# Optimization experiments

Measured on AMD Instinct MI355X. Metric: run time of the kernel, lower is better.

## Reference

```python
import jax, jax.numpy as jnp
import numpy as np

N = 64
EPS = 1e-4
N_ITER = 100
BRANCH = 10


def setup_inputs() -> dict:
    key = jax.random.key(0)
    x = jax.random.normal(key, (8192, 4096), dtype=jnp.float32)
    return {"x": x}


def _lml(x):
    # x: [n_batch, nx], nx > N assumed (as configured in setup_inputs)
    n_batch, nx = x.shape
    x_sorted = jnp.sort(x, axis=1)[:, ::-1]  # descending
    nu_lower = -x_sorted[:, N - 1] - 7.0  # [n_batch]
    nu_upper = -x_sorted[:, N] + 7.0      # [n_batch]
    ls = jnp.linspace(0.0, 1.0, BRANCH).astype(x.dtype)  # [branch]
    rows = jnp.arange(n_batch)

    def cond(state):
        i, lo, hi = state
        return (i < N_ITER) & jnp.any(hi - lo > EPS)

    def body(state):
        i, lo, hi = state
        r = hi - lo                     # [n_batch]
        I = r > EPS                     # rows still being refined
        nus = r[:, None] * ls + lo[:, None]  # [n_batch, branch]
        # sigmoid-sum constraint at each candidate nu: [n_batch, branch]
        fs = jax.nn.sigmoid(x[:, None, :] + nus[:, :, None]).sum(axis=2) - N
        neg = (fs < 0).sum(axis=1) - 1  # index of last negative iterate
        J = neg < 0                     # all-positive-iterates warning case
        i_lower = jnp.clip(neg, 0, BRANCH - 2)
        new_lo = nus[rows, i_lower]
        new_hi = nus[rows, i_lower + 1]
        new_lo = jnp.where(J, new_lo - 7.0, new_lo)
        lo = jnp.where(I, new_lo, lo)
        hi = jnp.where(I, new_hi, hi)
        return i + 1, lo, hi

    _, lo, hi = jax.lax.while_loop(cond, body, (0, nu_lower, nu_upper))
    nu = lo + (hi - lo) / 2.0
    return jax.nn.sigmoid(x + nu[:, None])


def reference(x):
    return _lml(x)
```

## Files before the change

### kernel.cpp

```cpp
#include <hip/hip_runtime.h>

#define ROWLEN 4096
#define TPB    256
#define LOG2E  1.44269504088896340736f

typedef float f32x4 __attribute__((ext_vector_type(4)));

__device__ __forceinline__ float exp2_fast(float x) {
    float r; asm("v_exp_f32 %0, %1" : "=v"(r) : "v"(x)); return r;
}
__device__ __forceinline__ float rcp_fast(float x) {
    float r; asm("v_rcp_f32 %0, %1" : "=v"(r) : "v"(x)); return r;
}
__device__ __forceinline__ float log2_fast(float x) {
    float r; asm("v_log_f32 %0, %1" : "=v"(r) : "v"(x)); return r;
}
__device__ __forceinline__ float sqrt_fast(float x) {
    float r; asm("v_sqrt_f32 %0, %1" : "=v"(r) : "v"(x)); return r;
}

__device__ __forceinline__ float sig_from(float v, float tnu) {
    float e = exp2_fast(fmaf(v, -LOG2E, tnu));
    return rcp_fast(1.0f + e);
}

__global__ __launch_bounds__(TPB) void lml_kernel(const float* __restrict__ x,
                                                  float* __restrict__ out) {
    const int lane = threadIdx.x & 63;
    const size_t row = (size_t)blockIdx.x * 4 + (threadIdx.x >> 6);
    const f32x4* __restrict__ rp = reinterpret_cast<const f32x4*>(x + row * ROWLEN);
    f32x4* __restrict__ op = reinterpret_cast<f32x4*>(out + row * ROWLEN);

    float v[64];
#pragma unroll
    for (int k = 0; k < 16; ++k) {
        f32x4 f = rp[k * 64 + lane];
        v[4*k+0] = f.x; v[4*k+1] = f.y; v[4*k+2] = f.z; v[4*k+3] = f.w;
    }

    float s10 = 0, s11 = 0, s12 = 0, s13 = 0;
    float s20 = 0, s21 = 0, s22 = 0, s23 = 0;
#pragma unroll
    for (int k = 0; k < 16; ++k) {
        float e0 = exp2_fast(v[4*k+0] * LOG2E);
        float e1 = exp2_fast(v[4*k+1] * LOG2E);
        float e2 = exp2_fast(v[4*k+2] * LOG2E);
        float e3 = exp2_fast(v[4*k+3] * LOG2E);
        s10 += e0; s11 += e1; s12 += e2; s13 += e3;
        s20 = fmaf(e0, e0, s20); s21 = fmaf(e1, e1, s21);
        s22 = fmaf(e2, e2, s22); s23 = fmaf(e3, e3, s23);
    }
    float S1 = (s10 + s11) + (s12 + s13);
    float S2 = (s20 + s21) + (s22 + s23);
#pragma unroll
    for (int off = 32; off >= 1; off >>= 1) {
        S1 += __shfl_xor(S1, off, 64);
        S2 += __shfl_xor(S2, off, 64);
    }

    float disc = fmaxf(fmaf(S1, S1, -256.0f * S2), 0.0f);
    float lo = (6.0f - log2_fast(S1)) * (1.0f / LOG2E);
    float hi = (7.0f - log2_fast(S1 + sqrt_fast(disc))) * (1.0f / LOG2E);
    float nu = 0.5f * (lo + hi);

#pragma unroll 1
    for (int it = 0; it < 2; ++it) {
        const float tnu = -LOG2E * nu;
        float a0 = 0, a1 = 0, a2 = 0, a3 = 0;
        float b0 = 0, b1 = 0, b2 = 0, b3 = 0;
#pragma unroll
        for (int k = 0; k < 16; ++k) {
            float x0 = sig_from(v[4*k+0], tnu);
            float x1 = sig_from(v[4*k+1], tnu);
            float x2 = sig_from(v[4*k+2], tnu);
            float x3 = sig_from(v[4*k+3], tnu);
            a0 += x0; a1 += x1; a2 += x2; a3 += x3;
            b0 = fmaf(x0, -x0, b0 + x0); b1 = fmaf(x1, -x1, b1 + x1);
            b2 = fmaf(x2, -x2, b2 + x2); b3 = fmaf(x3, -x3, b3 + x3);
        }
        float fs = (a0 + a1) + (a2 + a3);
        float fw = (b0 + b1) + (b2 + b3);
#pragma unroll
        for (int off = 32; off >= 1; off >>= 1) {
            fs += __shfl_xor(fs, off, 64);
            fw += __shfl_xor(fw, off, 64);
        }
        if (fs < 64.0f) lo = nu; else hi = nu;
        const float h = (log2_fast(fs) - 6.0f) * (1.0f / LOG2E);
        float nun = nu - h * fs * rcp_fast(fmaxf(fw, 1e-20f));
        if (!(nun > lo && nun < hi)) nun = 0.5f * (lo + hi);
        nu = nun;
    }

    const float tnu = -LOG2E * nu;
#pragma unroll
    for (int k = 0; k < 16; ++k) {
        f32x4 f;
        f.x = sig_from(v[4*k+0], tnu);
        f.y = sig_from(v[4*k+1], tnu);
        f.z = sig_from(v[4*k+2], tnu);
        f.w = sig_from(v[4*k+3], tnu);
        __builtin_nontemporal_store(f, op + k * 64 + lane);
    }
}

extern "C" void kernel_launch(void* const* d_in, const int* in_sizes, int n_in,
                              void* d_out, int out_size, void* d_ws, size_t ws_size,
                              hipStream_t stream) {
    const float* x = (const float*)d_in[0];
    float* out = (float*)d_out;
    const int rows = in_sizes[0] / ROWLEN;
    lml_kernel<<<rows / 4, TPB, 0, stream>>>(x, out);
}
```

Before: 235.2 us.

## Work in exp-domain with block-wide rows and double-buffered row loads

Each row is now handled by the full 256-thread block rather than by a single wave, with cross-wave reductions done through shared memory and barriers. Each thread keeps only 16 values per row, and the next row's load is issued while the current row is processed. The values are converted once to exp(x), so every sigmoid becomes u/(1+u) with u = e^x·t, which removes one exp per element in each Newton iteration and in the output pass. This lowers register pressure and raises occupancy. The cost is barrier synchronisation per row and a different bracketing scheme (an added min term for the upper bound), which changes the numerics.

```diff
diff --git a/kernel.cpp b/kernel.cpp
--- a/kernel.cpp
+++ b/kernel.cpp
@@ -2,106 +2,123 @@
 
 #define ROWLEN 4096
 #define TPB    256
+#define RPB    4
 #define LOG2E  1.44269504088896340736f
 
 typedef float f32x4 __attribute__((ext_vector_type(4)));
 
-__device__ __forceinline__ float exp2_fast(float x) {
-    float r; asm("v_exp_f32 %0, %1" : "=v"(r) : "v"(x)); return r;
-}
-__device__ __forceinline__ float rcp_fast(float x) {
-    float r; asm("v_rcp_f32 %0, %1" : "=v"(r) : "v"(x)); return r;
-}
-__device__ __forceinline__ float log2_fast(float x) {
-    float r; asm("v_log_f32 %0, %1" : "=v"(r) : "v"(x)); return r;
-}
-__device__ __forceinline__ float sqrt_fast(float x) {
-    float r; asm("v_sqrt_f32 %0, %1" : "=v"(r) : "v"(x)); return r;
+__device__ __forceinline__ float exp2_fast(float x){float r;asm("v_exp_f32 %0, %1":"=v"(r):"v"(x));return r;}
+__device__ __forceinline__ float rcp_fast (float x){float r;asm("v_rcp_f32 %0, %1":"=v"(r):"v"(x));return r;}
+__device__ __forceinline__ float log2_fast(float x){float r;asm("v_log_f32 %0, %1":"=v"(r):"v"(x));return r;}
+__device__ __forceinline__ float sqrt_fast(float x){float r;asm("v_sqrt_f32 %0, %1":"=v"(r):"v"(x));return r;}
+
+__device__ __forceinline__ void red_barrier() {
+    asm volatile("s_waitcnt lgkmcnt(0)" ::: "memory");
+    __builtin_amdgcn_s_barrier();
 }
 
-__device__ __forceinline__ float sig_from(float v, float tnu) {
-    float e = exp2_fast(fmaf(v, -LOG2E, tnu));
-    return rcp_fast(1.0f + e);
+__device__ __forceinline__ void load_row(const float* __restrict__ x, size_t row,
+                                         int t, float (&buf)[16]) {
+    const f32x4* rp = reinterpret_cast<const f32x4*>(x + row * ROWLEN);
+#pragma unroll
+    for (int k = 0; k < 4; ++k) {
+        f32x4 f = rp[k * TPB + t];
+        buf[4*k+0]=f.x; buf[4*k+1]=f.y; buf[4*k+2]=f.z; buf[4*k+3]=f.w;
+    }
 }
 
-__global__ __launch_bounds__(TPB) void lml_kernel(const float* __restrict__ x,
-                                                  float* __restrict__ out) {
-    const int lane = threadIdx.x & 63;
-    const size_t row = (size_t)blockIdx.x * 4 + (threadIdx.x >> 6);
-    const f32x4* __restrict__ rp = reinterpret_cast<const f32x4*>(x + row * ROWLEN);
-    f32x4* __restrict__ op = reinterpret_cast<f32x4*>(out + row * ROWLEN);
+__device__ __forceinline__ void process_row(float (&E)[16], float* __restrict__ outp,
+                                            int t, float (*red)[16], int rbase) {
+    const int lane = t & 63, wave = t >> 6;
 
-    float v[64];
+    float s1a=0, s1b=0, s2a=0, s2b=0, mna=3.4e38f, mnb=3.4e38f;
 #pragma unroll
-    for (int k = 0; k < 16; ++k) {
-        f32x4 f = rp[k * 64 + lane];
-        v[4*k+0] = f.x; v[4*k+1] = f.y; v[4*k+2] = f.z; v[4*k+3] = f.w;
+    for (int i = 0; i < 16; i += 2) {
+        float e0 = exp2_fast(E[i]   * LOG2E);
+        float e1 = exp2_fast(E[i+1] * LOG2E);
+        E[i] = e0; E[i+1] = e1;
+        s1a += e0; s1b += e1;
+        s2a = fmaf(e0, e0, s2a); s2b = fmaf(e1, e1, s2b);
+        mna = fminf(mna, e0);    mnb = fminf(mnb, e1);
     }
-
-    float s10 = 0, s11 = 0, s12 = 0, s13 = 0;
-    float s20 = 0, s21 = 0, s22 = 0, s23 = 0;
-#pragma unroll
-    for (int k = 0; k < 16; ++k) {
-        float e0 = exp2_fast(v[4*k+0] * LOG2E);
-        float e1 = exp2_fast(v[4*k+1] * LOG2E);
-        float e2 = exp2_fast(v[4*k+2] * LOG2E);
-        float e3 = exp2_fast(v[4*k+3] * LOG2E);
-        s10 += e0; s11 += e1; s12 += e2; s13 += e3;
-        s20 = fmaf(e0, e0, s20); s21 = fmaf(e1, e1, s21);
-        s22 = fmaf(e2, e2, s22); s23 = fmaf(e3, e3, s23);
-    }
-    float S1 = (s10 + s11) + (s12 + s13);
-    float S2 = (s20 + s21) + (s22 + s23);
+    float S1 = s1a + s1b, S2 = s2a + s2b, mn = fminf(mna, mnb);
 #pragma unroll
     for (int off = 32; off >= 1; off >>= 1) {
         S1 += __shfl_xor(S1, off, 64);
         S2 += __shfl_xor(S2, off, 64);
+        mn = fminf(mn, __shfl_xor(mn, off, 64));
+    }
+    if (lane == 0) { float* s = red[rbase] + wave * 4; s[0]=S1; s[1]=S2; s[2]=mn; }
+    red_barrier();
+    {
+        const float* s = red[rbase];
+        S1 = (s[0]+s[4]) + (s[8]+s[12]);
+        S2 = (s[1]+s[5]) + (s[9]+s[13]);
+        mn = fminf(fminf(s[2],s[6]), fminf(s[10],s[14]));
     }
 
-    float disc = fmaxf(fmaf(S1, S1, -256.0f * S2), 0.0f);
-    float lo = (6.0f - log2_fast(S1)) * (1.0f / LOG2E);
-    float hi = (7.0f - log2_fast(S1 + sqrt_fast(disc))) * (1.0f / LOG2E);
-    float nu = 0.5f * (lo + hi);
+    float disc = fmaf(S1, S1, -256.0f * S2);
+    float tl = 64.0f * rcp_fast(S1);
+    float th = (disc > 0.0f) ? 128.0f * rcp_fast(S1 + sqrt_fast(disc)) : rcp_fast(mn);
+    float tt = sqrt_fast(tl * th);
 
 #pragma unroll 1
     for (int it = 0; it < 2; ++it) {
-        const float tnu = -LOG2E * nu;
-        float a0 = 0, a1 = 0, a2 = 0, a3 = 0;
-        float b0 = 0, b1 = 0, b2 = 0, b3 = 0;
+        float fa=0, fb=0, wa=0, wb=0;
 #pragma unroll
-        for (int k = 0; k < 16; ++k) {
-            float x0 = sig_from(v[4*k+0], tnu);
-            float x1 = sig_from(v[4*k+1], tnu);
-            float x2 = sig_from(v[4*k+2], tnu);
-            float x3 = sig_from(v[4*k+3], tnu);
-            a0 += x0; a1 += x1; a2 += x2; a3 += x3;
-            b0 = fmaf(x0, -x0, b0 + x0); b1 = fmaf(x1, -x1, b1 + x1);
-            b2 = fmaf(x2, -x2, b2 + x2); b3 = fmaf(x3, -x3, b3 + x3);
+        for (int i = 0; i < 16; i += 2) {
+            float u0 = E[i] * tt,            u1 = E[i+1] * tt;
+            float r0 = rcp_fast(1.0f + u0),  r1 = rcp_fast(1.0f + u1);
+            float g0 = u0 * r0,              g1 = u1 * r1;
+            fa += g0; fb += g1;
+            wa = fmaf(g0, r0, wa); wb = fmaf(g1, r1, wb);
         }
-        float fs = (a0 + a1) + (a2 + a3);
-        float fw = (b0 + b1) + (b2 + b3);
+        float fs = fa + fb, fw = wa + wb;
 #pragma unroll
         for (int off = 32; off >= 1; off >>= 1) {
             fs += __shfl_xor(fs, off, 64);
             fw += __shfl_xor(fw, off, 64);
         }
-        if (fs < 64.0f) lo = nu; else hi = nu;
-        const float h = (log2_fast(fs) - 6.0f) * (1.0f / LOG2E);
-        float nun = nu - h * fs * rcp_fast(fmaxf(fw, 1e-20f));
-        if (!(nun > lo && nun < hi)) nun = 0.5f * (lo + hi);
-        nu = nun;
+        if (lane == 0) { float* s = red[rbase+1] + wave*4 + it*2; s[0]=fs; s[1]=fw; }
+        red_barrier();
+        {
+            const float* s = red[rbase+1] + it*2;
+            fs = (s[0]+s[4]) + (s[8]+s[12]);
+            fw = (s[1]+s[5]) + (s[9]+s[13]);
+        }
+        if (fs < 64.0f) tl = tt; else th = tt;
+        float step = (6.0f - log2_fast(fs)) * fs * rcp_fast(fw);
+        float tn = tt * exp2_fast(step);
+        tt = (tn > tl && tn < th) ? tn : sqrt_fast(tl * th);
     }
 
-    const float tnu = -LOG2E * nu;
 #pragma unroll
-    for (int k = 0; k < 16; ++k) {
+    for (int k = 0; k < 4; ++k) {
         f32x4 f;
-        f.x = sig_from(v[4*k+0], tnu);
-        f.y = sig_from(v[4*k+1], tnu);
-        f.z = sig_from(v[4*k+2], tnu);
-        f.w = sig_from(v[4*k+3], tnu);
-        __builtin_nontemporal_store(f, op + k * 64 + lane);
+#pragma unroll
+        for (int j = 0; j < 4; ++j) {
+            float u = E[4*k+j] * tt;
+            f[j] = u * rcp_fast(1.0f + u);
+        }
+        __builtin_nontemporal_store(f, reinterpret_cast<f32x4*>(outp) + k * TPB + t);
     }
+}
+
+__global__ __launch_bounds__(TPB) void lml_kernel(const float* __restrict__ x,
+                                                  float* __restrict__ out) {
+    const int t = threadIdx.x;
+    __shared__ float red[2 * RPB][16];
+    const size_t r0 = (size_t)blockIdx.x * RPB;
+    float A[16], B[16];
+
+    load_row(x, r0 + 0, t, A);
+    load_row(x, r0 + 1, t, B);
+    process_row(A, out + (r0 + 0) * ROWLEN, t, red, 0);
+    load_row(x, r0 + 2, t, A);
+    process_row(B, out + (r0 + 1) * ROWLEN, t, red, 2);
+    load_row(x, r0 + 3, t, B);
+    process_row(A, out + (r0 + 2) * ROWLEN, t, red, 4);
+    process_row(B, out + (r0 + 3) * ROWLEN, t, red, 6);
 }
 
 extern "C" void kernel_launch(void* const* d_in, const int* in_sizes, int n_in,
@@ -110,5 +127,5 @@
     const float* x = (const float*)d_in[0];
     float* out = (float*)d_out;
     const int rows = in_sizes[0] / ROWLEN;
-    lml_kernel<<<rows / 4, TPB, 0, stream>>>(x, out);
+    lml_kernel<<<rows / RPB, TPB, 0, stream>>>(x, out);
 }
```

Result: no change. 239.3 us (+1.7%).
